# Kernel optimization log

Hardware: AMD Instinct MI355X
Metric: run time of the kernel (lower is better)

## Reference

```python
import jax, jax.numpy as jnp
import numpy as np

N = 16384
C_IN = 128
C_OUT = 128
S_DIM = 4
P_DIM = 32
K = 16


def setup_inputs() -> dict:
    key = jax.random.key(0)
    ks = jax.random.split(key, 8)
    lim = lambda fan_in: 1.0 / np.sqrt(fan_in)
    u = lambda k_, shape, b: jax.random.uniform(k_, shape, jnp.float32, -b, b)
    return {
        "x": jax.random.normal(ks[0], (N, C_IN), jnp.float32),
        "Ws": u(ks[1], (S_DIM, C_IN), lim(C_IN)),
        "bs": u(ks[2], (S_DIM,), lim(C_IN)),
        "Wh": u(ks[3], (P_DIM, C_IN), lim(C_IN)),
        "bh": u(ks[4], (P_DIM,), lim(C_IN)),
        "W1": u(ks[5], (C_OUT, C_IN), lim(C_IN)),
        "W2": u(ks[6], (C_OUT, 2 * P_DIM), lim(2 * P_DIM)),
        "b2": u(ks[7], (C_OUT,), lim(2 * P_DIM)),
        "k": K,
    }


def reference(x, Ws, bs, Wh, bh, W1, W2, b2, k):
    # latent space positions and message vectors
    s = x @ Ws.T + bs            # [N, S]
    h = x @ Wh.T + bh            # [N, P]
    # squared-distance matrix via Gram trick (monotone in true distance,
    # so k-NN indices match torch.cdist + topk(largest=False))
    sq = jnp.sum(s * s, axis=-1)                         # [N]
    d2 = sq[:, None] + sq[None, :] - 2.0 * (s @ s.T)     # [N, N]
    _, idx = jax.lax.top_k(-d2, k)                       # [N, k] neighbour ids (incl. self)
    # exact squared latent distance to selected neighbours (as in torch code)
    s_j = s[idx]                                          # [N, k, S]
    w = jnp.exp(-10.0 * jnp.sum((s[:, None, :] - s_j) ** 2, axis=-1))  # [N, k]
    msg = h[idx] * w[..., None]                           # [N, k, P]
    agg = jnp.concatenate([msg.mean(axis=1), msg.max(axis=1)], axis=-1)  # [N, 2P]
    return x @ W1.T + agg @ W2.T + b2                     # [N, C_OUT]
```

## Files before the change

kernel.cpp:

```cpp
#include <hip/hip_runtime.h>
#include <hip/hip_bf16.h>


#define NPTS 16384
#define CIN  128
#define SD   4
#define PD   32
#define KNN  16
#define COUT 128
#define FLTMAX 3.4028234663852886e+38f
#define NBIN 33
#define QPB  8
#define QCAP 512
#define MCAP 128

typedef float v2f __attribute__((ext_vector_type(2)));
typedef unsigned int uint;
typedef unsigned long long u64;

#define WS_S4     0
#define WS_H      0x40000
#define WS_AGG_M  0x280000
#define WS_WT_M   0x680000
#define WS_T2     0x6A0000
#define WS_MASK   0x700000
#define WS_NEED_M 0x2700000
#define WS_CJ_F   0x400000
#define WS_AGG_F  0xC00000
#define WS_WT_F   0x1000000
#define JS   16
#define TJF  (NPTS/JS)

__device__ __forceinline__ float d2f(const float4 a, const float4 b) {
  v2f d0 = {a.x - b.x, a.y - b.y};
  v2f d1 = {a.z - b.z, a.w - b.w};
  v2f pr = d0*d0 + d1*d1;
  return pr.x + pr.y;
}

__global__ __launch_bounds__(256) void k1_proj(
    const float* __restrict__ x, const float* __restrict__ Ws, const float* __restrict__ bs,
    const float* __restrict__ Wh, const float* __restrict__ bh,
    float4* __restrict__ s4, float* __restrict__ h) {
  __shared__ float  lw[36*128];
  __shared__ float  lx[64*132];
  __shared__ double rs[3*64*5];
  __shared__ float  rh[3*64*33];
  const int t = threadIdx.x;
  const int row0 = blockIdx.x * 64;
  for (int i2 = t; i2 < 36*128; i2 += 256)
    lw[i2] = (i2 < 512) ? Ws[i2] : Wh[i2 - 512];
#pragma unroll
  for (int g = 0; g < 8; ++g) {
    int fi = g*256 + t;
    int r = fi >> 5, c4 = fi & 31;
    *(float4*)&lx[r*132 + c4*4] = *(const float4*)&x[(size_t)(row0 + r)*CIN + c4*4];
  }
  __syncthreads();
  const int kq = t >> 6;
  const int r  = t & 63;
  const int kb = kq * 32;
  double sacc[4] = {0.0, 0.0, 0.0, 0.0};
  float  hacc[32];
#pragma unroll
  for (int p = 0; p < 32; ++p) hacc[p] = 0.f;
#pragma unroll
  for (int k4 = 0; k4 < 8; ++k4) {
    float4 xv = *(const float4*)&lx[r*132 + kb + k4*4];
    int kg = kb + k4*4;
#pragma unroll
    for (int p = 0; p < 4; ++p) {
      float4 wv = *(const float4*)&lw[p*128 + kg];
      sacc[p] = fma((double)xv.x, (double)wv.x, sacc[p]);
      sacc[p] = fma((double)xv.y, (double)wv.y, sacc[p]);
      sacc[p] = fma((double)xv.z, (double)wv.z, sacc[p]);
      sacc[p] = fma((double)xv.w, (double)wv.w, sacc[p]);
    }
#pragma unroll
    for (int p = 0; p < 32; ++p) {
      float4 wv = *(const float4*)&lw[(4+p)*128 + kg];
      hacc[p] = fmaf(xv.x, wv.x, fmaf(xv.y, wv.y, fmaf(xv.z, wv.z, fmaf(xv.w, wv.w, hacc[p]))));
    }
  }
  if (kq > 0) {
    const int bq = kq - 1;
#pragma unroll
    for (int d = 0; d < 4; ++d) rs[(bq*64 + r)*5 + d] = sacc[d];
#pragma unroll
    for (int p = 0; p < 32; ++p) rh[(bq*64 + r)*33 + p] = hacc[p];
  }
  __syncthreads();
  if (kq == 0) {
    const int row = row0 + r;
    float so[4];
#pragma unroll
    for (int d = 0; d < 4; ++d) {
      double sd = sacc[d] + rs[(0*64 + r)*5 + d] + rs[(1*64 + r)*5 + d]
                + rs[(2*64 + r)*5 + d] + (double)bs[d];
      so[d] = (float)sd;
    }
    s4[row] = make_float4(so[0], so[1], so[2], so[3]);
#pragma unroll
    for (int p4 = 0; p4 < 8; ++p4) {
      float o[4];
#pragma unroll
      for (int c = 0; c < 4; ++c) {
        int p = p4*4 + c;
        o[c] = hacc[p] + rh[(0*64 + r)*33 + p] + rh[(1*64 + r)*33 + p]
             + rh[(2*64 + r)*33 + p] + bh[p];
      }
      *(float4*)&h[(size_t)row*PD + p4*4] = make_float4(o[0], o[1], o[2], o[3]);
    }
  }
}

__global__ __launch_bounds__(256) void k2t_thresh(
    const float4* __restrict__ s4, float* __restrict__ t2) {
  __shared__ float4 tile[2064];
  __shared__ uint   lhist[256*NBIN];
  const int t = threadIdx.x;
#pragma unroll
  for (int g = 0; g < 8; ++g) {
    int j = g*256 + t;
    tile[j + (j >> 7)] = s4[j];
  }
#pragma unroll
  for (int b = 0; b < NBIN; ++b) lhist[t*NBIN + b] = 0u;
  const int ql = t >> 4, tq = t & 15;
  const int q  = blockIdx.x*16 + ql;
  const float4 sq = s4[q];
  __syncthreads();
  float tau = d2f(sq, tile[tq*129]);
#pragma unroll
  for (int m = 1; m < 16; m <<= 1) tau = fmaxf(tau, __shfl_xor(tau, m, 16));
  const int ktop = (int)(__float_as_uint(tau) >> 21);
  const int hb = t*NBIN;
#pragma unroll 4
  for (int u = 0; u < 128; ++u) {
    float4 p = tile[tq*129 + u];
    float e = d2f(sq, p);
    int key = (int)(__float_as_uint(e) >> 21);
    int rel = ktop - key;
    rel = rel < 0 ? 0 : (rel > 32 ? 32 : rel);
    atomicAdd(&lhist[hb + rel], 1u);
  }
  __syncthreads();
  uint c0 = 0, c1 = 0;
  const int qb = ql*16;
  for (int u = 0; u < 16; ++u) {
    c0 += lhist[(qb + u)*NBIN + tq*2];
    c1 += (tq*2 + 1 < NBIN) ? lhist[(qb + u)*NBIN + tq*2 + 1] : 0u;
  }
  int S = (int)(c0 + c1);
#pragma unroll
  for (int d = 1; d < 16; d <<= 1) {
    int v = __shfl_down(S, d, 16);
    S += (tq + d < 16) ? v : 0;
  }
  int g = -1;
  if (S >= KNN) g = 2*tq;
  if (S - (int)c0 >= KNN) g = 2*tq + 1;
#pragma unroll
  for (int m = 1; m < 16; m <<= 1) g = max(g, __shfl_xor(g, m, 16));
  if (tq == 0) {
    uint K = (uint)(ktop - g);
    t2[q] = __uint_as_float((K << 21) | 0x1FFFFFu);
  }
}

__global__ __launch_bounds__(256) void k2b_mask(
    const float4* __restrict__ s4, const float* __restrict__ t2, uint4* __restrict__ maskw) {
  __shared__ float4 tile4[128];
  __shared__ float  tileb[128];
  const int t  = threadIdx.x;
  const int c  = blockIdx.x >> 4;
  const int ig = blockIdx.x & 15;
  if (t < 128) {
    float4 p = s4[c*128 + t];
    tile4[t] = p;
    tileb[t] = 0.5f*(p.x*p.x + p.y*p.y + p.z*p.z + p.w*p.w);
  }
  const int q0 = ig*1024 + t;
  float4 sq[4]; float ui[4];
#pragma unroll
  for (int m = 0; m < 4; ++m) {
    int q = q0 + m*256;
    float4 s = s4[q];
    sq[m] = s;
    float n2 = s.x*s.x + s.y*s.y + s.z*s.z + s.w*s.w;
    ui[m] = 0.5f*(n2 - t2[q]) - 4e-6f;
  }
  __syncthreads();
  uint msk[4][4];
#pragma unroll 1
  for (int w = 0; w < 4; ++w) {
    uint mk0 = 0u, mk1 = 0u, mk2 = 0u, mk3 = 0u;
#pragma unroll
    for (int bit = 31; bit >= 0; --bit) {
      float4 p = tile4[w*32 + bit];
      float nb = tileb[w*32 + bit];
      float a0 = fmaf(sq[0].x, p.x, fmaf(sq[0].y, p.y, fmaf(sq[0].z, p.z, fmaf(sq[0].w, p.w, -nb))));
      float a1 = fmaf(sq[1].x, p.x, fmaf(sq[1].y, p.y, fmaf(sq[1].z, p.z, fmaf(sq[1].w, p.w, -nb))));
      float a2 = fmaf(sq[2].x, p.x, fmaf(sq[2].y, p.y, fmaf(sq[2].z, p.z, fmaf(sq[2].w, p.w, -nb))));
      float a3 = fmaf(sq[3].x, p.x, fmaf(sq[3].y, p.y, fmaf(sq[3].z, p.z, fmaf(sq[3].w, p.w, -nb))));
      mk0 = mk0 + mk0 + (a0 >= ui[0] ? 1u : 0u);
      mk1 = mk1 + mk1 + (a1 >= ui[1] ? 1u : 0u);
      mk2 = mk2 + mk2 + (a2 >= ui[2] ? 1u : 0u);
      mk3 = mk3 + mk3 + (a3 >= ui[3] ? 1u : 0u);
    }
    msk[0][w] = mk0; msk[1][w] = mk1; msk[2][w] = mk2; msk[3][w] = mk3;
  }
#pragma unroll
  for (int m = 0; m < 4; ++m) {
    int q = q0 + m*256;
    maskw[(size_t)c*NPTS + q] = make_uint4(msk[m][0], msk[m][1], msk[m][2], msk[m][3]);
  }
}

__global__ __launch_bounds__(256) void k3_sel2(
    const float4* __restrict__ s4, const float* __restrict__ h,
    const uint4* __restrict__ maskw, float* __restrict__ agg) {
  __shared__ u64  qbuf[QPB*MCAP];
  __shared__ u64  keys[QPB*QCAP];
  __shared__ u64  win[QPB*KNN];
  __shared__ uint hist[QPB*32];
  __shared__ uint cnts[QPB];
  __shared__ uint mc[QPB];
  unsigned short* jl = (unsigned short*)qbuf;
  const int t  = threadIdx.x;
  const int ql = t >> 5, ln = t & 31;
  const int q  = blockIdx.x*QPB + ql;
  if (ln == 0) { cnts[ql] = 0u; mc[ql] = 0u; }
  hist[ql*32 + ln] = 0u;
  if (ln < KNN) win[ql*KNN + ln] = 0ull;
  const float4 sq = s4[q];
  __syncthreads();
  uint wv[16]; int pc = 0;
#pragma unroll
  for (int u = 0; u < 4; ++u) {
    const int c = ln*4 + u;
    uint4 m4 = maskw[(size_t)c*NPTS + q];
    wv[u*4+0] = m4.x; wv[u*4+1] = m4.y; wv[u*4+2] = m4.z; wv[u*4+3] = m4.w;
    pc += __popc(m4.x) + __popc(m4.y) + __popc(m4.z) + __popc(m4.w);
  }
  int base = (int)atomicAdd(&cnts[ql], (uint)pc);
#pragma unroll
  for (int w = 0; w < 16; ++w) {
    uint bits = wv[w];
    const int jb = (ln*4 + (w >> 2))*128 + (w & 3)*32;
    while (bits) {
      int b = __builtin_ctz(bits); bits &= bits - 1;
      if (base < QCAP) jl[ql*QCAP + base] = (unsigned short)(jb + b);
      ++base;
    }
  }
  __syncthreads();
  const int cnt = min((int)cnts[ql], QCAP);
  uint kmax = 0u;
  for (int u = ln; u < cnt; u += 32) {
    int j = jl[ql*QCAP + u];
    float e = d2f(sq, s4[j]);
    uint db = __float_as_uint(e);
    keys[ql*QCAP + u] = ((u64)db << 14) | (uint)j;
    kmax = max(kmax, db >> 21);
  }
#pragma unroll
  for (int m = 1; m < 32; m <<= 1) kmax = max(kmax, (uint)__shfl_xor((int)kmax, m, 32));
  for (int u = ln; u < cnt; u += 32) {
    uint cls = (uint)(keys[ql*QCAP + u] >> 35);
    uint rel = min(kmax - cls, 31u);
    atomicAdd(&hist[ql*32 + rel], 1u);
  }
  __syncthreads();
  uint cum = hist[ql*32 + ln];
#pragma unroll
  for (int d = 1; d < 32; d <<= 1) {
    uint v = (uint)__shfl_down((int)cum, d, 32);
    if (ln + d < 32) cum += v;
  }
  const uint need = (uint)(cnt < KNN ? cnt : KNN);
  u64 bal = __ballot(cum >= need);
  uint half = (uint)(bal >> (((t >> 5) & 1) * 32));
  const uint rstar = 31u - (uint)__builtin_clz(half);
  const uint bcls = kmax - rstar;
  __syncthreads();
  for (int u = ln; u < cnt; u += 32) {
    u64 key = keys[ql*QCAP + u];
    if ((uint)(key >> 35) <= bcls) {
      uint pos = atomicAdd(&mc[ql], 1u);
      if (pos < MCAP) qbuf[ql*MCAP + pos] = key;
    }
  }
  __syncthreads();
  const int mcnt = (int)mc[ql];
  if (mcnt <= MCAP) {
    for (int w = ln; w < mcnt; w += 32) {
      u64 key = qbuf[ql*MCAP + w];
      int rank = 0;
      for (int v = 0; v < mcnt; ++v) rank += (qbuf[ql*MCAP + v] < key) ? 1 : 0;
      if (rank < KNN) win[ql*KNN + rank] = key;
    }
  } else {
    for (int u = ln; u < cnt; u += 32) {
      u64 key = keys[ql*QCAP + u];
      if ((uint)(key >> 35) <= bcls) {
        int rank = 0;
        for (int v = 0; v < cnt; ++v) rank += (keys[ql*QCAP + v] < key) ? 1 : 0;
        if (rank < KNN) win[ql*KNN + rank] = key;
      }
    }
  }
  __syncthreads();
  float sum = 0.f, mx = -FLTMAX;
#pragma unroll 1
  for (int r = 0; r < KNN; ++r) {
    u64 key = win[ql*KNN + r];
    float d2 = __uint_as_float((uint)(key >> 14));
    int j = (int)(key & 16383u);
    float w = __expf(-10.f * d2);
    float m = w * h[(size_t)j*PD + ln];
    sum += m; mx = fmaxf(mx, m);
  }
  agg[(size_t)q*64 + ln]      = sum * 0.0625f;
  agg[(size_t)q*64 + 32 + ln] = mx;
}

__global__ __launch_bounds__(256) void k2_knn_fb(
    const float4* __restrict__ s4, unsigned short* __restrict__ cand_j) {
  __shared__ float4 tile[TJF];
  __shared__ int    lbuf[256*33];
  const int t  = threadIdx.x;
  const int ib = blockIdx.x & 31;
  const int jc = blockIdx.x >> 5;
  const int jbase = jc * TJF;
#pragma unroll
  for (int g = 0; g < 4; ++g) tile[g*256 + t] = s4[jbase + g*256 + t];
  const int ia = ib*256 + t;
  const int ic = ia + 8192;
  const float4 sa = s4[ia];
  const float4 sc = s4[ic];
  __syncthreads();
  float va[KNN], vb[KNN]; int ja[KNN], jb[KNN];
#pragma unroll
  for (int q = 0; q < KNN; ++q) { va[q] = FLTMAX; ja[q] = 0; vb[q] = FLTMAX; jb[q] = 0; }
  float cma = FLTMAX, cmb = FLTMAX;
  int cpa = 0, cpb = 0, ca = 0, cb = 0;
  auto insertA = [&](float e, int jj) {
#pragma unroll
    for (int q = 0; q < KNN; ++q) if (q == cpa) { va[q] = e; ja[q] = jj; }
    cma = va[0]; cpa = 0;
#pragma unroll
    for (int q = 1; q < KNN; ++q) { if (va[q] > cma) { cma = va[q]; cpa = q; } }
  };
  auto insertB = [&](float e, int jj) {
#pragma unroll
    for (int q = 0; q < KNN; ++q) if (q == cpb) { vb[q] = e; jb[q] = jj; }
    cmb = vb[0]; cpb = 0;
#pragma unroll
    for (int q = 1; q < KNN; ++q) { if (vb[q] > cmb) { cmb = vb[q]; cpb = q; } }
  };
  auto compactA = [&]() {
    for (int u = 0; u < ca; ++u) {
      int jj = lbuf[t*33 + u];
      float e = d2f(sa, tile[jj]);
      if (e < cma) insertA(e, jj);
    }
    ca = 0;
  };
  auto compactB = [&]() {
    for (int u = 0; u < cb; ++u) {
      int jj = lbuf[t*33 + 16 + u];
      float e = d2f(sc, tile[jj]);
      if (e < cmb) insertB(e, jj);
    }
    cb = 0;
  };
  for (int ob = 0; ob < TJF/8; ++ob) {
#pragma unroll
    for (int u = 0; u < 8; ++u) {
      int jj = ob*8 + u;
      float4 p = tile[jj];
      float ea = d2f(sa, p);
      float eb = d2f(sc, p);
      if (ea < cma) { lbuf[t*33 + ca] = jj; ++ca; }
      if (eb < cmb) { lbuf[t*33 + 16 + cb] = jj; ++cb; }
    }
    if (__any(ca > 8)) compactA();
    if (__any(cb > 8)) compactB();
  }
  compactA(); compactB();
#pragma unroll
  for (int q = 0; q < KNN; ++q) {
    int c = jc*KNN + q;
    cand_j[(size_t)c*NPTS + ia] = (unsigned short)(ja[q] + jbase);
    cand_j[(size_t)c*NPTS + ic] = (unsigned short)(jb[q] + jbase);
  }
}

__global__ __launch_bounds__(256) void k3_merge_fb(
    const float4* __restrict__ s4, const float4* __restrict__ h4,
    const unsigned short* __restrict__ cand_j, float* __restrict__ agg) {
  __shared__ float le[64*67];
  __shared__ int   lj[64*67];
  const int t  = threadIdx.x;
  const int il = t & 63, tq = t >> 6;
  const int i  = blockIdx.x*64 + il;
  const float4 si = s4[i];
  float val[KNN]; int vid[KNN];
#pragma unroll
  for (int q = 0; q < KNN; ++q) { val[q] = FLTMAX; vid[q] = 0; }
  float cmax = FLTMAX; int cpos = 0;
  for (int u = 0; u < 64; ++u) {
    int c = tq*64 + u;
    int j = cand_j[(size_t)c*NPTS + i];
    float e = d2f(si, s4[j]);
    if (e < cmax) {
#pragma unroll
      for (int q = 0; q < KNN; ++q) if (q == cpos) { val[q] = e; vid[q] = j; }
      cmax = val[0]; cpos = 0;
#pragma unroll
      for (int q = 1; q < KNN; ++q) { if (val[q] > cmax) { cmax = val[q]; cpos = q; } }
    }
  }
#pragma unroll
  for (int q = 0; q < KNN; ++q) {
    le[il*67 + tq*16 + q] = val[q];
    lj[il*67 + tq*16 + q] = vid[q];
  }
  __syncthreads();
  if (t < 64) {
    float mv[KNN]; int mj[KNN];
#pragma unroll
    for (int q = 0; q < KNN; ++q) { mv[q] = FLTMAX; mj[q] = 0; }
    float cm2 = FLTMAX; int cp2 = 0;
    for (int u = 0; u < 64; ++u) {
      float e = le[t*67 + u];
      int   j = lj[t*67 + u];
      if (e < cm2) {
#pragma unroll
        for (int q = 0; q < KNN; ++q) if (q == cp2) { mv[q] = e; mj[q] = j; }
        cm2 = mv[0]; cp2 = 0;
#pragma unroll
        for (int q = 1; q < KNN; ++q) { if (mv[q] > cm2) { cm2 = mv[q]; cp2 = q; } }
      }
    }
#pragma unroll
    for (int q = 0; q < KNN; ++q) {
      le[t*67 + q] = __expf(-10.f * mv[q]);
      lj[t*67 + q] = mj[q];
    }
  }
  __syncthreads();
  float ms[8], mm[8];
#pragma unroll
  for (int p = 0; p < 8; ++p) { ms[p] = 0.f; mm[p] = -FLTMAX; }
#pragma unroll 1
  for (int q = 0; q < KNN; ++q) {
    float w = le[il*67 + q];
    int   j = lj[il*67 + q];
    float4 a = h4[(size_t)j*8 + tq*2];
    float4 b = h4[(size_t)j*8 + tq*2 + 1];
    float m0 = a.x*w, m1 = a.y*w, m2 = a.z*w, m3 = a.w*w;
    float m4 = b.x*w, m5 = b.y*w, m6 = b.z*w, m7 = b.w*w;
    ms[0] += m0; mm[0] = fmaxf(mm[0], m0);
    ms[1] += m1; mm[1] = fmaxf(mm[1], m1);
    ms[2] += m2; mm[2] = fmaxf(mm[2], m2);
    ms[3] += m3; mm[3] = fmaxf(mm[3], m3);
    ms[4] += m4; mm[4] = fmaxf(mm[4], m4);
    ms[5] += m5; mm[5] = fmaxf(mm[5], m5);
    ms[6] += m6; mm[6] = fmaxf(mm[6], m6);
    ms[7] += m7; mm[7] = fmaxf(mm[7], m7);
  }
  float4 o0 = make_float4(ms[0]*0.0625f, ms[1]*0.0625f, ms[2]*0.0625f, ms[3]*0.0625f);
  float4 o1 = make_float4(ms[4]*0.0625f, ms[5]*0.0625f, ms[6]*0.0625f, ms[7]*0.0625f);
  *(float4*)&agg[(size_t)i*64 + tq*8]      = o0;
  *(float4*)&agg[(size_t)i*64 + tq*8 + 4]  = o1;
  *(float4*)&agg[(size_t)i*64 + 32 + tq*8]     = make_float4(mm[0], mm[1], mm[2], mm[3]);
  *(float4*)&agg[(size_t)i*64 + 32 + tq*8 + 4] = make_float4(mm[4], mm[5], mm[6], mm[7]);
}

__global__ __launch_bounds__(256) void k4a_wt(
    const float* __restrict__ W1, const float* __restrict__ W2, float* __restrict__ wT) {
  int idx = blockIdx.x*256 + threadIdx.x;
  if (idx >= 192*COUT) return;
  int k = idx >> 7, c = idx & 127;
  float v = (k < 128) ? W1[(size_t)c*128 + k] : W2[(size_t)c*64 + (k - 128)];
  wT[(size_t)k*COUT + c] = v;
}

__global__ __launch_bounds__(256) void k4_out2(
    const float* __restrict__ x, const float* __restrict__ agg,
    const float* __restrict__ wT, const float* __restrict__ b2,
    float* __restrict__ out) {
  __shared__ float xa[32*192];
  const int t = threadIdx.x;
  const int row0 = blockIdx.x * 32;
#pragma unroll
  for (int g = 0; g < 4; ++g) {
    int fi = g*256 + t;
    int r = fi >> 5, c4 = fi & 31;
    *(float4*)&xa[r*192 + c4*4] = *(const float4*)&x[(size_t)(row0+r)*CIN + c4*4];
  }
#pragma unroll
  for (int g = 0; g < 2; ++g) {
    int fi = g*256 + t;
    int r = fi >> 4, c4 = fi & 15;
    *(float4*)&xa[r*192 + 128 + c4*4] = *(const float4*)&agg[(size_t)(row0+r)*64 + c4*4];
  }
  __syncthreads();
  const int c4 = t & 31;
  const int rg = t >> 5;
  float acc[4][4];
#pragma unroll
  for (int r = 0; r < 4; ++r) { acc[r][0]=0.f; acc[r][1]=0.f; acc[r][2]=0.f; acc[r][3]=0.f; }
  for (int k = 0; k < 192; k += 4) {
    float4 w0 = *(const float4*)&wT[(size_t)(k+0)*COUT + c4*4];
    float4 w1 = *(const float4*)&wT[(size_t)(k+1)*COUT + c4*4];
    float4 w2 = *(const float4*)&wT[(size_t)(k+2)*COUT + c4*4];
    float4 w3 = *(const float4*)&wT[(size_t)(k+3)*COUT + c4*4];
#pragma unroll
    for (int r = 0; r < 4; ++r) {
      float4 xv = *(const float4*)&xa[(rg*4 + r)*192 + k];
      acc[r][0] = fmaf(xv.x, w0.x, fmaf(xv.y, w1.x, fmaf(xv.z, w2.x, fmaf(xv.w, w3.x, acc[r][0]))));
      acc[r][1] = fmaf(xv.x, w0.y, fmaf(xv.y, w1.y, fmaf(xv.z, w2.y, fmaf(xv.w, w3.y, acc[r][1]))));
      acc[r][2] = fmaf(xv.x, w0.z, fmaf(xv.y, w1.z, fmaf(xv.z, w2.z, fmaf(xv.w, w3.z, acc[r][2]))));
      acc[r][3] = fmaf(xv.x, w0.w, fmaf(xv.y, w1.w, fmaf(xv.z, w2.w, fmaf(xv.w, w3.w, acc[r][3]))));
    }
  }
  float4 bias = *(const float4*)&b2[c4*4];
#pragma unroll
  for (int r = 0; r < 4; ++r) {
    float4 o = make_float4(acc[r][0]+bias.x, acc[r][1]+bias.y, acc[r][2]+bias.z, acc[r][3]+bias.w);
    *(float4*)&out[(size_t)(row0 + rg*4 + r)*COUT + c4*4] = o;
  }
}

extern "C" void kernel_launch(void* const* d_in, const int* in_sizes, int n_in,
                              void* d_out, int out_size, void* d_ws, size_t ws_size,
                              hipStream_t stream) {
  const float* x  = (const float*)d_in[0];
  const float* Ws = (const float*)d_in[1];
  const float* bs = (const float*)d_in[2];
  const float* Wh = (const float*)d_in[3];
  const float* bh = (const float*)d_in[4];
  const float* W1 = (const float*)d_in[5];
  const float* W2 = (const float*)d_in[6];
  const float* b2 = (const float*)d_in[7];
  float* out = (float*)d_out;

  char* ws = (char*)d_ws;
  float4* s4 = (float4*)(ws + WS_S4);
  float*  h  = (float*) (ws + WS_H);

  k1_proj<<<NPTS/64, 256, 0, stream>>>(x, Ws, bs, Wh, bh, s4, h);

  if (ws_size >= (size_t)WS_NEED_M) {
    float* t2  = (float*)(ws + WS_T2);
    float* agg = (float*)(ws + WS_AGG_M);
    float* wT  = (float*)(ws + WS_WT_M);
    uint4* mw  = (uint4*)(ws + WS_MASK);
    k2t_thresh<<<NPTS/16, 256, 0, stream>>>(s4, t2);
    k2b_mask<<<2048, 256, 0, stream>>>(s4, t2, mw);
    k3_sel2<<<NPTS/QPB, 256, 0, stream>>>(s4, h, (const uint4*)mw, agg);
    k4a_wt<<<(192*COUT + 255)/256, 256, 0, stream>>>(W1, W2, wT);
    k4_out2<<<NPTS/32, 256, 0, stream>>>(x, agg, wT, b2, out);
  } else {
    unsigned short* cj = (unsigned short*)(ws + WS_CJ_F);
    float* agg = (float*)(ws + WS_AGG_F);
    float* wT  = (float*)(ws + WS_WT_F);
    k2_knn_fb<<<512, 256, 0, stream>>>(s4, cj);
    k3_merge_fb<<<NPTS/64, 256, 0, stream>>>(s4, (const float4*)h, cj, agg);
    k4a_wt<<<(192*COUT + 255)/256, 256, 0, stream>>>(W1, W2, wT);
    k4_out2<<<NPTS/32, 256, 0, stream>>>(x, agg, wT, b2, out);
  }
}
```

Measured before the change: 217.0 us.

## Pack mask-kernel math into float2 vector ops and coalesce mask reads

The mask kernel now handles 8 queries per thread instead of 4, with half as many blocks. It packs pairs of queries into float2 vectors so the distance FMAs can use packed fp32 instructions, and it writes each 32-bit mask word as soon as it is computed. The selection kernel changes how threads map to queries and chunks so that the 8 queries of a block are read together, giving more coalesced mask loads. This costs extra register pressure and scattered 4-byte mask stores.

```diff
diff --git a/kernel.cpp b/kernel.cpp
--- a/kernel.cpp
+++ b/kernel.cpp
@@ -169,51 +169,58 @@
 }
 
 __global__ __launch_bounds__(256) void k2b_mask(
-    const float4* __restrict__ s4, const float* __restrict__ t2, uint4* __restrict__ maskw) {
+    const float4* __restrict__ s4, const float* __restrict__ t2, uint* __restrict__ maskwu) {
   __shared__ float4 tile4[128];
   __shared__ float  tileb[128];
   const int t  = threadIdx.x;
-  const int c  = blockIdx.x >> 4;
-  const int ig = blockIdx.x & 15;
+  const int c  = blockIdx.x >> 3;
+  const int ig = blockIdx.x & 7;
   if (t < 128) {
     float4 p = s4[c*128 + t];
     tile4[t] = p;
     tileb[t] = 0.5f*(p.x*p.x + p.y*p.y + p.z*p.z + p.w*p.w);
   }
-  const int q0 = ig*1024 + t;
-  float4 sq[4]; float ui[4];
-#pragma unroll
-  for (int m = 0; m < 4; ++m) {
-    int q = q0 + m*256;
-    float4 s = s4[q];
-    sq[m] = s;
-    float n2 = s.x*s.x + s.y*s.y + s.z*s.z + s.w*s.w;
-    ui[m] = 0.5f*(n2 - t2[q]) - 4e-6f;
-  }
-  __syncthreads();
-  uint msk[4][4];
+  const int q0 = ig*2048 + t;
+  v2f qx[4], qy[4], qz[4], qw[4], uu[4];
+#pragma unroll
+  for (int pr = 0; pr < 4; ++pr) {
+    int qa = q0 + (2*pr)*256, qb = q0 + (2*pr+1)*256;
+    float4 sa = s4[qa], sb = s4[qb];
+    float na  = sa.x*sa.x + sa.y*sa.y + sa.z*sa.z + sa.w*sa.w;
+    float nbq = sb.x*sb.x + sb.y*sb.y + sb.z*sb.z + sb.w*sb.w;
+    qx[pr] = (v2f){sa.x, sb.x};
+    qy[pr] = (v2f){sa.y, sb.y};
+    qz[pr] = (v2f){sa.z, sb.z};
+    qw[pr] = (v2f){sa.w, sb.w};
+    uu[pr] = (v2f){0.5f*(na - t2[qa]) - 4e-6f, 0.5f*(nbq - t2[qb]) - 4e-6f};
+  }
+  __syncthreads();
 #pragma unroll 1
   for (int w = 0; w < 4; ++w) {
-    uint mk0 = 0u, mk1 = 0u, mk2 = 0u, mk3 = 0u;
+    uint mk[8];
+#pragma unroll
+    for (int m = 0; m < 8; ++m) mk[m] = 0u;
 #pragma unroll
     for (int bit = 31; bit >= 0; --bit) {
       float4 p = tile4[w*32 + bit];
       float nb = tileb[w*32 + bit];
-      float a0 = fmaf(sq[0].x, p.x, fmaf(sq[0].y, p.y, fmaf(sq[0].z, p.z, fmaf(sq[0].w, p.w, -nb))));
-      float a1 = fmaf(sq[1].x, p.x, fmaf(sq[1].y, p.y, fmaf(sq[1].z, p.z, fmaf(sq[1].w, p.w, -nb))));
-      float a2 = fmaf(sq[2].x, p.x, fmaf(sq[2].y, p.y, fmaf(sq[2].z, p.z, fmaf(sq[2].w, p.w, -nb))));
-      float a3 = fmaf(sq[3].x, p.x, fmaf(sq[3].y, p.y, fmaf(sq[3].z, p.z, fmaf(sq[3].w, p.w, -nb))));
-      mk0 = mk0 + mk0 + (a0 >= ui[0] ? 1u : 0u);
-      mk1 = mk1 + mk1 + (a1 >= ui[1] ? 1u : 0u);
-      mk2 = mk2 + mk2 + (a2 >= ui[2] ? 1u : 0u);
-      mk3 = mk3 + mk3 + (a3 >= ui[3] ? 1u : 0u);
-    }
-    msk[0][w] = mk0; msk[1][w] = mk1; msk[2][w] = mk2; msk[3][w] = mk3;
-  }
-#pragma unroll
-  for (int m = 0; m < 4; ++m) {
-    int q = q0 + m*256;
-    maskw[(size_t)c*NPTS + q] = make_uint4(msk[m][0], msk[m][1], msk[m][2], msk[m][3]);
+      v2f px = {p.x, p.x}, py = {p.y, p.y}, pz = {p.z, p.z}, pw = {p.w, p.w};
+      v2f nn = {-nb, -nb};
+#pragma unroll
+      for (int pr = 0; pr < 4; ++pr) {
+        v2f a = qw[pr]*pw + nn;
+        a = qz[pr]*pz + a;
+        a = qy[pr]*py + a;
+        a = qx[pr]*px + a;
+        mk[2*pr]   = mk[2*pr]   + mk[2*pr]   + (a.x >= uu[pr].x ? 1u : 0u);
+        mk[2*pr+1] = mk[2*pr+1] + mk[2*pr+1] + (a.y >= uu[pr].y ? 1u : 0u);
+      }
+    }
+#pragma unroll
+    for (int m = 0; m < 8; ++m) {
+      int q = q0 + m*256;
+      maskwu[((size_t)c*NPTS + q)*4 + w] = mk[m];
+    }
   }
 }
 
@@ -235,22 +242,24 @@
   if (ln < KNN) win[ql*KNN + ln] = 0ull;
   const float4 sq = s4[q];
   __syncthreads();
+  const int qa = t & 7;
+  const int cg = t >> 3;
   uint wv[16]; int pc = 0;
 #pragma unroll
   for (int u = 0; u < 4; ++u) {
-    const int c = ln*4 + u;
-    uint4 m4 = maskw[(size_t)c*NPTS + q];
+    const int c = cg + u*32;
+    uint4 m4 = maskw[(size_t)c*NPTS + blockIdx.x*QPB + qa];
     wv[u*4+0] = m4.x; wv[u*4+1] = m4.y; wv[u*4+2] = m4.z; wv[u*4+3] = m4.w;
     pc += __popc(m4.x) + __popc(m4.y) + __popc(m4.z) + __popc(m4.w);
   }
-  int base = (int)atomicAdd(&cnts[ql], (uint)pc);
+  int base = (int)atomicAdd(&cnts[qa], (uint)pc);
 #pragma unroll
   for (int w = 0; w < 16; ++w) {
     uint bits = wv[w];
-    const int jb = (ln*4 + (w >> 2))*128 + (w & 3)*32;
+    const int jb = (cg + (w >> 2)*32)*128 + (w & 3)*32;
     while (bits) {
       int b = __builtin_ctz(bits); bits &= bits - 1;
-      if (base < QCAP) jl[ql*QCAP + base] = (unsigned short)(jb + b);
+      if (base < QCAP) jl[qa*QCAP + base] = (unsigned short)(jb + b);
       ++base;
     }
   }
@@ -558,9 +567,9 @@
     float* t2  = (float*)(ws + WS_T2);
     float* agg = (float*)(ws + WS_AGG_M);
     float* wT  = (float*)(ws + WS_WT_M);
-    uint4* mw  = (uint4*)(ws + WS_MASK);
+    uint*  mw  = (uint*)(ws + WS_MASK);
     k2t_thresh<<<NPTS/16, 256, 0, stream>>>(s4, t2);
-    k2b_mask<<<2048, 256, 0, stream>>>(s4, t2, mw);
+    k2b_mask<<<1024, 256, 0, stream>>>(s4, t2, mw);
     k3_sel2<<<NPTS/QPB, 256, 0, stream>>>(s4, h, (const uint4*)mw, agg);
     k4a_wt<<<(192*COUT + 255)/256, 256, 0, stream>>>(W1, W2, wT);
     k4_out2<<<NPTS/32, 256, 0, stream>>>(x, agg, wT, b2, out);
```

Result: no change. 219.2 us (+1.0%).

## Compute kNN candidate filter with bf16 split-precision MFMA and compacted lists

Applied to the files above, without the earlier changes.

Replaces the scalar FMA bitmask kernel with a matrix-core kernel. Each point's coordinates, norms and threshold are split into hi/lo bf16 pairs and packed so that one 16x16x32 MFMA produces the thresholded squared-distance test. Passing candidates are appended straight into per-query global index lists via atomics, which removes the bitmask write and read and the bit-unpacking in the selection kernel. The selection kernel also drops several __syncthreads, since each wavefront's work is now local. Risks: bf16 split precision with an epsilon pad could admit or miss borderline candidates, and the global atomics may contend.

```diff
diff --git a/kernel.cpp b/kernel.cpp
--- a/kernel.cpp
+++ b/kernel.cpp
@@ -13,17 +13,24 @@
 #define QPB  8
 #define QCAP 512
 #define MCAP 128
+#define EPAD 1e-3f
 
 typedef float v2f __attribute__((ext_vector_type(2)));
 typedef unsigned int uint;
 typedef unsigned long long u64;
+typedef unsigned short u16;
+typedef __attribute__((ext_vector_type(8))) short bf16x8;
+typedef __attribute__((ext_vector_type(4))) float f32x4;
 
 #define WS_S4     0
 #define WS_H      0x40000
 #define WS_AGG_M  0x280000
 #define WS_WT_M   0x680000
 #define WS_T2     0x6A0000
-#define WS_MASK   0x700000
+#define WS_SA     0x6B0000
+#define WS_SB     0x730000
+#define WS_CNT    0x7B0000
+#define WS_JL     0x7C0000
 #define WS_NEED_M 0x2700000
 #define WS_CJ_F   0x400000
 #define WS_AGG_F  0xC00000
@@ -36,6 +43,15 @@
   v2f d1 = {a.z - b.z, a.w - b.w};
   v2f pr = d0*d0 + d1*d1;
   return pr.x + pr.y;
+}
+
+__device__ __forceinline__ u16 f2bf(float x) {
+  uint u = __float_as_uint(x);
+  uint r = (u + 0x7FFFu + ((u >> 16) & 1u)) >> 16;
+  return (u16)r;
+}
+__device__ __forceinline__ float bf2f(u16 h) {
+  return __uint_as_float(((uint)h) << 16);
 }
 
 __global__ __launch_bounds__(256) void k1_proj(
@@ -168,97 +184,111 @@
   }
 }
 
-__global__ __launch_bounds__(256) void k2b_mask(
-    const float4* __restrict__ s4, const float* __restrict__ t2, uint4* __restrict__ maskw) {
-  __shared__ float4 tile4[128];
-  __shared__ float  tileb[128];
+__global__ __launch_bounds__(256) void k1b_pack(
+    const float4* __restrict__ s4, const float* __restrict__ t2,
+    uint4* __restrict__ sA, uint4* __restrict__ sB, uint* __restrict__ cnt) {
+  const int i = blockIdx.x*256 + threadIdx.x;
+  const float4 s = s4[i];
+  float sv[4] = {s.x, s.y, s.z, s.w};
+  const float n2 = s.x*s.x + s.y*s.y + s.z*s.z + s.w*s.w;
+  u16 hb[4], lb[4];
+#pragma unroll
+  for (int d = 0; d < 4; ++d) {
+    u16 hh = f2bf(sv[d]);
+    hb[d] = hh;
+    lb[d] = f2bf(sv[d] - bf2f(hh));
+  }
+  const float aq = -0.5f*(n2 - t2[i]) + EPAD;
+  const float bn = -0.5f*n2;
+  u16 aqh = f2bf(aq); u16 aql = f2bf(aq - bf2f(aqh));
+  u16 bnh = f2bf(bn); u16 bnl = f2bf(bn - bf2f(bnh));
+  const uint oneone = 0x3F803F80u;
+  uint a0 = (uint)hb[0] | ((uint)hb[1] << 16);
+  uint a1 = (uint)hb[2] | ((uint)hb[3] << 16);
+  uint l0 = (uint)lb[0] | ((uint)lb[1] << 16);
+  uint l1 = (uint)lb[2] | ((uint)lb[3] << 16);
+  uint aqw = (uint)aqh | ((uint)aql << 16);
+  uint bnw = (uint)bnh | ((uint)bnl << 16);
+  uint4 A0; A0.x = a0; A0.y = a1; A0.z = a0; A0.w = a1;
+  uint4 A1; A1.x = l0; A1.y = l1; A1.z = oneone; A1.w = aqw;
+  uint4 B0; B0.x = a0; B0.y = a1; B0.z = l0; B0.w = l1;
+  uint4 B1; B1.x = a0; B1.y = a1; B1.z = bnw; B1.w = oneone;
+  sA[(size_t)i*2]     = A0;
+  sA[(size_t)i*2 + 1] = A1;
+  sB[(size_t)i*2]     = B0;
+  sB[(size_t)i*2 + 1] = B1;
+  cnt[i] = 0u;
+}
+
+__global__ __launch_bounds__(256) void k2b_mfma(
+    const u16* __restrict__ sA, const u16* __restrict__ sB,
+    uint* __restrict__ cnt, u16* __restrict__ jl) {
+  __shared__ uint4 lBv[512];
+  u16* lB = (u16*)lBv;
   const int t  = threadIdx.x;
-  const int c  = blockIdx.x >> 4;
-  const int ig = blockIdx.x & 15;
-  if (t < 128) {
-    float4 p = s4[c*128 + t];
-    tile4[t] = p;
-    tileb[t] = 0.5f*(p.x*p.x + p.y*p.y + p.z*p.z + p.w*p.w);
-  }
-  const int q0 = ig*1024 + t;
-  float4 sq[4]; float ui[4];
-#pragma unroll
-  for (int m = 0; m < 4; ++m) {
-    int q = q0 + m*256;
-    float4 s = s4[q];
-    sq[m] = s;
-    float n2 = s.x*s.x + s.y*s.y + s.z*s.z + s.w*s.w;
-    ui[m] = 0.5f*(n2 - t2[q]) - 4e-6f;
-  }
-  __syncthreads();
-  uint msk[4][4];
+  const int wv = t >> 6, ln = t & 63;
+  const int lr = ln & 15, lk = ln >> 4;
+  const int qb = (blockIdx.x >> 4) * 256 + wv * 64;
+  const int j0 = (blockIdx.x & 15) * 1024;
+  const bf16x8 zf = {0,0,0,0,0,0,0,0};
+  bf16x8 afr[4];
+#pragma unroll
+  for (int m = 0; m < 4; ++m)
+    afr[m] = (lk < 2) ? *(const bf16x8*)&sA[(size_t)(qb + m*16 + lr)*16 + lk*8] : zf;
 #pragma unroll 1
-  for (int w = 0; w < 4; ++w) {
-    uint mk0 = 0u, mk1 = 0u, mk2 = 0u, mk3 = 0u;
-#pragma unroll
-    for (int bit = 31; bit >= 0; --bit) {
-      float4 p = tile4[w*32 + bit];
-      float nb = tileb[w*32 + bit];
-      float a0 = fmaf(sq[0].x, p.x, fmaf(sq[0].y, p.y, fmaf(sq[0].z, p.z, fmaf(sq[0].w, p.w, -nb))));
-      float a1 = fmaf(sq[1].x, p.x, fmaf(sq[1].y, p.y, fmaf(sq[1].z, p.z, fmaf(sq[1].w, p.w, -nb))));
-      float a2 = fmaf(sq[2].x, p.x, fmaf(sq[2].y, p.y, fmaf(sq[2].z, p.z, fmaf(sq[2].w, p.w, -nb))));
-      float a3 = fmaf(sq[3].x, p.x, fmaf(sq[3].y, p.y, fmaf(sq[3].z, p.z, fmaf(sq[3].w, p.w, -nb))));
-      mk0 = mk0 + mk0 + (a0 >= ui[0] ? 1u : 0u);
-      mk1 = mk1 + mk1 + (a1 >= ui[1] ? 1u : 0u);
-      mk2 = mk2 + mk2 + (a2 >= ui[2] ? 1u : 0u);
-      mk3 = mk3 + mk3 + (a3 >= ui[3] ? 1u : 0u);
-    }
-    msk[0][w] = mk0; msk[1][w] = mk1; msk[2][w] = mk2; msk[3][w] = mk3;
-  }
-#pragma unroll
-  for (int m = 0; m < 4; ++m) {
-    int q = q0 + m*256;
-    maskw[(size_t)c*NPTS + q] = make_uint4(msk[m][0], msk[m][1], msk[m][2], msk[m][3]);
+  for (int jc = 0; jc < 4; ++jc) {
+    __syncthreads();
+    {
+      const uint4* src = (const uint4*)&sB[(size_t)(j0 + jc*256 + t)*16];
+      uint4 v0 = src[0], v1 = src[1];
+      lBv[t*2]     = v0;
+      lBv[t*2 + 1] = v1;
+    }
+    __syncthreads();
+#pragma unroll 1
+    for (int jt = 0; jt < 16; ++jt) {
+      const bf16x8 bfr = (lk < 2) ? *(const bf16x8*)&lB[(jt*16 + lr)*16 + lk*8] : zf;
+      const int jcol = j0 + jc*256 + jt*16 + lr;
+#pragma unroll
+      for (int m = 0; m < 4; ++m) {
+        f32x4 acc = {0.f, 0.f, 0.f, 0.f};
+        acc = __builtin_amdgcn_mfma_f32_16x16x32_bf16(afr[m], bfr, acc, 0, 0, 0);
+        float mx = fmaxf(fmaxf(acc[0], acc[1]), fmaxf(acc[2], acc[3]));
+        if (__any(mx >= 0.f)) {
+          const int qq = qb + m*16 + lk*4;
+#pragma unroll
+          for (int i = 0; i < 4; ++i) {
+            if (acc[i] >= 0.f) {
+              uint pos = atomicAdd(&cnt[qq + i], 1u);
+              if (pos < QCAP) jl[(size_t)(qq + i)*QCAP + pos] = (u16)jcol;
+            }
+          }
+        }
+      }
+    }
   }
 }
 
 __global__ __launch_bounds__(256) void k3_sel2(
     const float4* __restrict__ s4, const float* __restrict__ h,
-    const uint4* __restrict__ maskw, float* __restrict__ agg) {
+    const uint* __restrict__ cntg, const u16* __restrict__ jlg,
+    float* __restrict__ agg) {
   __shared__ u64  qbuf[QPB*MCAP];
   __shared__ u64  keys[QPB*QCAP];
   __shared__ u64  win[QPB*KNN];
   __shared__ uint hist[QPB*32];
-  __shared__ uint cnts[QPB];
   __shared__ uint mc[QPB];
-  unsigned short* jl = (unsigned short*)qbuf;
   const int t  = threadIdx.x;
   const int ql = t >> 5, ln = t & 31;
   const int q  = blockIdx.x*QPB + ql;
-  if (ln == 0) { cnts[ql] = 0u; mc[ql] = 0u; }
+  if (ln == 0) mc[ql] = 0u;
   hist[ql*32 + ln] = 0u;
   if (ln < KNN) win[ql*KNN + ln] = 0ull;
   const float4 sq = s4[q];
-  __syncthreads();
-  uint wv[16]; int pc = 0;
-#pragma unroll
-  for (int u = 0; u < 4; ++u) {
-    const int c = ln*4 + u;
-    uint4 m4 = maskw[(size_t)c*NPTS + q];
-    wv[u*4+0] = m4.x; wv[u*4+1] = m4.y; wv[u*4+2] = m4.z; wv[u*4+3] = m4.w;
-    pc += __popc(m4.x) + __popc(m4.y) + __popc(m4.z) + __popc(m4.w);
-  }
-  int base = (int)atomicAdd(&cnts[ql], (uint)pc);
-#pragma unroll
-  for (int w = 0; w < 16; ++w) {
-    uint bits = wv[w];
-    const int jb = (ln*4 + (w >> 2))*128 + (w & 3)*32;
-    while (bits) {
-      int b = __builtin_ctz(bits); bits &= bits - 1;
-      if (base < QCAP) jl[ql*QCAP + base] = (unsigned short)(jb + b);
-      ++base;
-    }
-  }
-  __syncthreads();
-  const int cnt = min((int)cnts[ql], QCAP);
+  const int cnt = min((int)cntg[q], QCAP);
   uint kmax = 0u;
   for (int u = ln; u < cnt; u += 32) {
-    int j = jl[ql*QCAP + u];
+    int j = jlg[(size_t)q*QCAP + u];
     float e = d2f(sq, s4[j]);
     uint db = __float_as_uint(e);
     keys[ql*QCAP + u] = ((u64)db << 14) | (uint)j;
@@ -271,7 +301,6 @@
     uint rel = min(kmax - cls, 31u);
     atomicAdd(&hist[ql*32 + rel], 1u);
   }
-  __syncthreads();
   uint cum = hist[ql*32 + ln];
 #pragma unroll
   for (int d = 1; d < 32; d <<= 1) {
@@ -283,7 +312,6 @@
   uint half = (uint)(bal >> (((t >> 5) & 1) * 32));
   const uint rstar = 31u - (uint)__builtin_clz(half);
   const uint bcls = kmax - rstar;
-  __syncthreads();
   for (int u = ln; u < cnt; u += 32) {
     u64 key = keys[ql*QCAP + u];
     if ((uint)(key >> 35) <= bcls) {
@@ -291,7 +319,6 @@
       if (pos < MCAP) qbuf[ql*MCAP + pos] = key;
     }
   }
-  __syncthreads();
   const int mcnt = (int)mc[ql];
   if (mcnt <= MCAP) {
     for (int w = ln; w < mcnt; w += 32) {
@@ -310,7 +337,6 @@
       }
     }
   }
-  __syncthreads();
   float sum = 0.f, mx = -FLTMAX;
 #pragma unroll 1
   for (int r = 0; r < KNN; ++r) {
@@ -558,10 +584,14 @@
     float* t2  = (float*)(ws + WS_T2);
     float* agg = (float*)(ws + WS_AGG_M);
     float* wT  = (float*)(ws + WS_WT_M);
-    uint4* mw  = (uint4*)(ws + WS_MASK);
+    uint4* sa  = (uint4*)(ws + WS_SA);
+    uint4* sb  = (uint4*)(ws + WS_SB);
+    uint*  cnt = (uint*) (ws + WS_CNT);
+    u16*   jl  = (u16*)  (ws + WS_JL);
     k2t_thresh<<<NPTS/16, 256, 0, stream>>>(s4, t2);
-    k2b_mask<<<2048, 256, 0, stream>>>(s4, t2, mw);
-    k3_sel2<<<NPTS/QPB, 256, 0, stream>>>(s4, h, (const uint4*)mw, agg);
+    k1b_pack<<<NPTS/256, 256, 0, stream>>>(s4, t2, sa, sb, cnt);
+    k2b_mfma<<<1024, 256, 0, stream>>>((const u16*)sa, (const u16*)sb, cnt, jl);
+    k3_sel2<<<NPTS/QPB, 256, 0, stream>>>(s4, h, cnt, jl, agg);
     k4a_wt<<<(192*COUT + 255)/256, 256, 0, stream>>>(W1, W2, wT);
     k4_out2<<<NPTS/32, 256, 0, stream>>>(x, agg, wT, b2, out);
   } else {
```

New measurement: 403.5 us. 1.86x slower.
